# Kernel optimization log

Measured on AMD Instinct MI355X. Metric: run time of the kernel, lower is better.

The kernel has to match this reference:

```python
import jax, jax.numpy as jnp
import numpy as np

C = 128      # in channels
CO = 64      # out channels
G = 32       # group-norm groups
RES_IN = 32  # input resolution
RES_OUT = 64 # subdivided resolution
N = 20000    # active input voxels
EPS = 1e-5


def setup_inputs() -> dict:
    key = jax.random.key(0)
    ks = jax.random.split(key, 12)
    # unique active voxel coords at RES_IN (batch index 0, single instance)
    rng = np.random.default_rng(0)
    flat = rng.choice(RES_IN ** 3, size=N, replace=False)
    xyz = np.stack([flat // (RES_IN * RES_IN), (flat // RES_IN) % RES_IN, flat % RES_IN], axis=1)
    x_coords = jnp.asarray(np.concatenate([np.zeros((N, 1), np.int32), xyz.astype(np.int32)], axis=1))
    x_feats = jax.random.normal(ks[0], (N, C), dtype=jnp.float32)
    gn1_g = 1.0 + 0.1 * jax.random.normal(ks[1], (C,), dtype=jnp.float32)
    gn1_b = 0.1 * jax.random.normal(ks[2], (C,), dtype=jnp.float32)
    W1 = 0.05 * jax.random.normal(ks[3], (3, 3, 3, C, CO), dtype=jnp.float32)
    b1 = 0.01 * jax.random.normal(ks[4], (CO,), dtype=jnp.float32)
    gn2_g = 1.0 + 0.1 * jax.random.normal(ks[5], (CO,), dtype=jnp.float32)
    gn2_b = 0.1 * jax.random.normal(ks[6], (CO,), dtype=jnp.float32)
    W2 = 0.05 * jax.random.normal(ks[7], (3, 3, 3, CO, CO), dtype=jnp.float32)  # zero_module in source; random here to exercise math
    b2 = 0.01 * jax.random.normal(ks[8], (CO,), dtype=jnp.float32)
    Ws = 0.05 * jax.random.normal(ks[9], (C, CO), dtype=jnp.float32)   # 1x1 skip conv
    bs = 0.01 * jax.random.normal(ks[10], (CO,), dtype=jnp.float32)
    return dict(x_feats=x_feats, x_coords=x_coords, gn1_g=gn1_g, gn1_b=gn1_b,
                W1=W1, b1=b1, gn2_g=gn2_g, gn2_b=gn2_b, W2=W2, b2=b2, Ws=Ws, bs=bs)


def group_norm(f, g, b):
    # single-instance sparse group norm: stats per group over all points
    n, c = f.shape
    x = f.reshape(n, G, c // G)
    mu = jnp.mean(x, axis=(0, 2), keepdims=True)
    var = jnp.mean((x - mu) ** 2, axis=(0, 2), keepdims=True)
    return ((x - mu) * jax.lax.rsqrt(var + EPS)).reshape(n, c) * g + b


def subdivide(coords, feats):
    n = coords.shape[0]
    offs = jnp.stack(jnp.meshgrid(jnp.arange(2), jnp.arange(2), jnp.arange(2), indexing='ij'), -1).reshape(8, 3)
    xyz = coords[:, None, 1:] * 2 + offs[None].astype(coords.dtype)          # [n,8,3]
    bidx = jnp.broadcast_to(coords[:, None, :1], (n, 8, 1))
    new_coords = jnp.concatenate([bidx, xyz], axis=-1).reshape(n * 8, 4)
    return new_coords, jnp.repeat(feats, 8, axis=0)


def subm_conv3(coords, feats, W, b):
    # submanifold 3x3x3 sparse conv: scatter to padded dense grid, gather 27 neighbors per active site
    cin = feats.shape[1]
    grid = jnp.zeros((RES_OUT + 2, RES_OUT + 2, RES_OUT + 2, cin), feats.dtype)
    grid = grid.at[coords[:, 1] + 1, coords[:, 2] + 1, coords[:, 3] + 1].set(feats)
    acc = jnp.zeros((feats.shape[0], W.shape[-1]), feats.dtype)
    for i in range(3):
        for j in range(3):
            for k in range(3):
                nb = grid[coords[:, 1] + i, coords[:, 2] + j, coords[:, 3] + k]  # [n, cin]
                acc = acc + nb @ W[i, j, k]
    return acc + b


def reference(x_feats, x_coords, gn1_g, gn1_b, W1, b1, gn2_g, gn2_b, W2, b2, Ws, bs):
    h = jax.nn.silu(group_norm(x_feats, gn1_g, gn1_b))
    hc, hf = subdivide(x_coords, h)
    _, xf = subdivide(x_coords, x_feats)
    hf = subm_conv3(hc, hf, W1, b1)
    hf = jax.nn.silu(group_norm(hf, gn2_g, gn2_b))
    hf = subm_conv3(hc, hf, W2, b2)
    out = hf + (xf @ Ws + bs)  # residual + 1x1 skip conv (out_channels != channels)
    return out
```

## Files before the change

### kernel.cpp

```cpp
#include <hip/hip_runtime.h>
#include <hip/hip_bf16.h>
#include <math.h>

#define N_PTS 20000
#define C_IN 128
#define C_OUT 64
#define M_PTS (N_PTS*8)
#define EPS 1e-5f

typedef __attribute__((ext_vector_type(8))) short short8;
typedef __attribute__((ext_vector_type(4))) float float4v;

__device__ __forceinline__ ushort f2bf(float f){
    unsigned int i = __float_as_uint(f);
    unsigned int r = i + 0x7fffu + ((i >> 16) & 1u);
    return (ushort)(r >> 16);
}
__device__ __forceinline__ float bf2f(ushort u){ return __uint_as_float(((unsigned int)u) << 16); }
__device__ __forceinline__ float silu(float z){ return z / (1.f + expf(-z)); }


__global__ void __launch_bounds__(256) prep_kernel(
    const float* __restrict__ W1, const float* __restrict__ W2,
    ushort* __restrict__ Wt1, ushort* __restrict__ Wt2,
    int* __restrict__ pg, ushort* __restrict__ h, ushort* __restrict__ h2,
    const float* __restrict__ x, float* __restrict__ stats)
{
    const int b = blockIdx.x, tid = threadIdx.x;
    if (b < 864){
        int idx = b * 256 + tid;
        int j = idx & 7, l = (idx >> 3) & 63, nb = (idx >> 9) & 3, kb = (idx >> 11) & 3, t = idx >> 13;
        int ci = kb * 32 + (l >> 4) * 8 + j, co = nb * 16 + (l & 15);
        Wt1[idx] = f2bf(W1[(t * C_IN + ci) * 64 + co]);
    } else if (b < 1296){
        int idx = (b - 864) * 256 + tid;
        int j = idx & 7, l = (idx >> 3) & 63, nb = (idx >> 9) & 3, kb = (idx >> 11) & 1, t = idx >> 12;
        int ci = kb * 32 + (l >> 4) * 8 + j, co = nb * 16 + (l & 15);
        Wt2[idx] = f2bf(W2[(t * C_OUT + ci) * 64 + co]);
    } else if (b < 1424){
        int i = (b - 1296) * 256 + tid;
        pg[i] = -1;
        if (b == 1296){
            if (tid < C_IN) h[(size_t)N_PTS * C_IN + tid] = 0;
            if (tid < C_OUT) h2[(size_t)M_PTS * C_OUT + tid] = 0;
        }
    } else {
        __shared__ float ls[64];
        if (tid < 64) ls[tid] = 0.f;
        __syncthreads();
        const int g = tid & 31;
        const int r0 = (b - 1424) * 8 + (tid >> 5);
        float sum = 0.f, sq = 0.f;
        for (int r = r0; r < N_PTS; r += 4096){
            float4 v = *(const float4*)(x + (size_t)r * C_IN + g * 4);
            sum += v.x + v.y + v.z + v.w;
            sq  += v.x*v.x + v.y*v.y + v.z*v.z + v.w*v.w;
        }
        atomicAdd(&ls[g], sum);
        atomicAdd(&ls[32 + g], sq);
        __syncthreads();
        if (tid < 64) atomicAdd(&stats[tid], ls[tid]);
    }
}

__global__ void __launch_bounds__(256) mid_kernel(
    const int* __restrict__ cds, int* __restrict__ pg,
    const float* __restrict__ x, const float* __restrict__ stats,
    const float* __restrict__ g1, const float* __restrict__ b1, ushort* __restrict__ h,
    const float* __restrict__ Wsk, const float* __restrict__ bsk, float* __restrict__ s)
{
    __shared__ float w[C_IN * C_OUT];
    const int b = blockIdx.x, tid = threadIdx.x;
    if (b < 79){
        int i = b * 256 + tid;
        if (i < N_PTS){
            const int* cd = cds + i * 4;
            pg[(cd[1] * 32 + cd[2]) * 32 + cd[3]] = i;
        }
    } else if (b < 2579){
        int i = ((b - 79) * 256 + tid) * 4;
        int c0 = i & (C_IN - 1);
        int g = c0 >> 2;
        float mu = stats[g] * (1.0f / (N_PTS * 4.0f));
        float var = stats[32 + g] * (1.0f / (N_PTS * 4.0f)) - mu * mu;
        float rs = rsqrtf(var + EPS);
        float4 v = *(const float4*)(x + i);
        ushort4 o;
        o.x = f2bf(silu((v.x - mu) * rs * g1[c0+0] + b1[c0+0]));
        o.y = f2bf(silu((v.y - mu) * rs * g1[c0+1] + b1[c0+1]));
        o.z = f2bf(silu((v.z - mu) * rs * g1[c0+2] + b1[c0+2]));
        o.w = f2bf(silu((v.w - mu) * rs * g1[c0+3] + b1[c0+3]));
        *(ushort4*)(h + i) = o;
    } else {
        for (int j = tid; j < C_IN * C_OUT; j += 256) w[j] = Wsk[j];
        __syncthreads();
        int co = tid & 63, pr = tid >> 6;
        int p = (b - 2579) * 4 + pr;
        const float* xr = x + (size_t)p * C_IN;
        float a = bsk[co];
        for (int cb = 0; cb < C_IN; cb += 4){
            float4 v = *(const float4*)(xr + cb);
            a += v.x * w[(cb+0)*64+co] + v.y * w[(cb+1)*64+co]
               + v.z * w[(cb+2)*64+co] + v.w * w[(cb+3)*64+co];
        }
        s[(size_t)p * C_OUT + co] = a;
    }
}

template<int CIN, int CHILD>
__global__ void __launch_bounds__(64, 3) conv_direct(
    const ushort* __restrict__ feat, const int* __restrict__ pg,
    const int* __restrict__ coords, const ushort* __restrict__ Wt,
    const float* __restrict__ bias, const float* __restrict__ skip,
    ushort* __restrict__ hf1_bf, float* __restrict__ out, float* __restrict__ statsAcc)
{
    constexpr int KB = CIN / 32;
    __shared__ int rws[64];
    const int l = threadIdx.x;
    const int r16 = l & 15, qd = l >> 4;
    const int mb = blockIdx.x * 64;

    int cx0, cy0, cz0;
    {
        int m = mb + l, p = m >> 3, o = m & 7;
        cx0 = 2 * coords[p*4+1] + ((o >> 2) & 1);
        cy0 = 2 * coords[p*4+2] + ((o >> 1) & 1);
        cz0 = 2 * coords[p*4+3] + (o & 1);
    }

    float4v acc[4][4];
#pragma unroll
    for (int rb = 0; rb < 4; rb++)
#pragma unroll
        for (int nb = 0; nb < 4; nb++)
#pragma unroll
            for (int rg = 0; rg < 4; rg++) acc[rb][nb][rg] = 0.f;

    for (int t = 0; t < 27; t++){
        const int dx = t / 9 - 1, dy = (t / 3) % 3 - 1, dz = t % 3 - 1;
        const int cx = cx0 + dx, cy = cy0 + dy, cz = cz0 + dz;
        int row = 8 * N_PTS;
        if ((unsigned)cx < 64u && (unsigned)cy < 64u && (unsigned)cz < 64u){
            int pidx = pg[((cx >> 1) * 32 + (cy >> 1)) * 32 + (cz >> 1)];
            if (pidx >= 0) row = pidx * 8 + (((cx & 1) << 2) | ((cy & 1) << 1) | (cz & 1));
        }
        rws[l] = row;
        __syncthreads();
        int fr0 = rws[r16], fr1 = rws[16 + r16], fr2 = rws[32 + r16], fr3 = rws[48 + r16];
        if (!CHILD){ fr0 >>= 3; fr1 >>= 3; fr2 >>= 3; fr3 >>= 3; }
        const ushort* a0 = feat + (size_t)fr0 * CIN + qd * 8;
        const ushort* a1 = feat + (size_t)fr1 * CIN + qd * 8;
        const ushort* a2 = feat + (size_t)fr2 * CIN + qd * 8;
        const ushort* a3 = feat + (size_t)fr3 * CIN + qd * 8;
        const ushort* wt = Wt + (size_t)t * (KB * 2048) + l * 8;
#pragma unroll
        for (int kb = 0; kb < KB; kb++){
            short8 b0 = *(const short8*)(wt + (kb*4+0)*512);
            short8 b1 = *(const short8*)(wt + (kb*4+1)*512);
            short8 b2 = *(const short8*)(wt + (kb*4+2)*512);
            short8 b3 = *(const short8*)(wt + (kb*4+3)*512);
            short8 av0 = *(const short8*)(a0 + kb*32);
            short8 av1 = *(const short8*)(a1 + kb*32);
            short8 av2 = *(const short8*)(a2 + kb*32);
            short8 av3 = *(const short8*)(a3 + kb*32);
            acc[0][0] = __builtin_amdgcn_mfma_f32_16x16x32_bf16(av0, b0, acc[0][0], 0, 0, 0);
            acc[0][1] = __builtin_amdgcn_mfma_f32_16x16x32_bf16(av0, b1, acc[0][1], 0, 0, 0);
            acc[0][2] = __builtin_amdgcn_mfma_f32_16x16x32_bf16(av0, b2, acc[0][2], 0, 0, 0);
            acc[0][3] = __builtin_amdgcn_mfma_f32_16x16x32_bf16(av0, b3, acc[0][3], 0, 0, 0);
            acc[1][0] = __builtin_amdgcn_mfma_f32_16x16x32_bf16(av1, b0, acc[1][0], 0, 0, 0);
            acc[1][1] = __builtin_amdgcn_mfma_f32_16x16x32_bf16(av1, b1, acc[1][1], 0, 0, 0);
            acc[1][2] = __builtin_amdgcn_mfma_f32_16x16x32_bf16(av1, b2, acc[1][2], 0, 0, 0);
            acc[1][3] = __builtin_amdgcn_mfma_f32_16x16x32_bf16(av1, b3, acc[1][3], 0, 0, 0);
            acc[2][0] = __builtin_amdgcn_mfma_f32_16x16x32_bf16(av2, b0, acc[2][0], 0, 0, 0);
            acc[2][1] = __builtin_amdgcn_mfma_f32_16x16x32_bf16(av2, b1, acc[2][1], 0, 0, 0);
            acc[2][2] = __builtin_amdgcn_mfma_f32_16x16x32_bf16(av2, b2, acc[2][2], 0, 0, 0);
            acc[2][3] = __builtin_amdgcn_mfma_f32_16x16x32_bf16(av2, b3, acc[2][3], 0, 0, 0);
            acc[3][0] = __builtin_amdgcn_mfma_f32_16x16x32_bf16(av3, b0, acc[3][0], 0, 0, 0);
            acc[3][1] = __builtin_amdgcn_mfma_f32_16x16x32_bf16(av3, b1, acc[3][1], 0, 0, 0);
            acc[3][2] = __builtin_amdgcn_mfma_f32_16x16x32_bf16(av3, b2, acc[3][2], 0, 0, 0);
            acc[3][3] = __builtin_amdgcn_mfma_f32_16x16x32_bf16(av3, b3, acc[3][3], 0, 0, 0);
        }
    }

    float bsv[4] = { bias[r16], bias[16 + r16], bias[32 + r16], bias[48 + r16] };
    if (!CHILD){
        float ps[4] = {0,0,0,0}, pq[4] = {0,0,0,0};
#pragma unroll
        for (int rb = 0; rb < 4; rb++)
#pragma unroll
            for (int nb = 0; nb < 4; nb++)
#pragma unroll
                for (int rg = 0; rg < 4; rg++){
                    int mm = mb + rb * 16 + qd * 4 + rg;
                    float v = acc[rb][nb][rg] + bsv[nb];
                    hf1_bf[(size_t)mm * 64 + nb * 16 + r16] = f2bf(v);
                    ps[nb] += v; pq[nb] += v * v;
                }
#pragma unroll
        for (int nb = 0; nb < 4; nb++){
            float s1 = ps[nb], s2 = pq[nb];
            s1 += __shfl_xor(s1, 16, 64); s2 += __shfl_xor(s2, 16, 64);
            s1 += __shfl_xor(s1, 32, 64); s2 += __shfl_xor(s2, 32, 64);
            if (qd == 0){
                atomicAdd(&statsAcc[64 + nb * 16 + r16], s1);
                atomicAdd(&statsAcc[128 + nb * 16 + r16], s2);
            }
        }
    } else {
#pragma unroll
        for (int rb = 0; rb < 4; rb++)
#pragma unroll
            for (int rg = 0; rg < 4; rg++){
                int mm = mb + rb * 16 + qd * 4 + rg;
                const float* sk = skip + (size_t)(mm >> 3) * 64;
#pragma unroll
                for (int nb = 0; nb < 4; nb++){
                    int co = nb * 16 + r16;
                    out[(size_t)mm * 64 + co] = acc[rb][nb][rg] + bsv[nb] + sk[co];
                }
            }
    }
}

__global__ void __launch_bounds__(256) h2_kernel(
    const ushort* __restrict__ hf1, const float* __restrict__ stats,
    const float* __restrict__ gg, const float* __restrict__ gb, ushort* __restrict__ h2)
{
    int i = (blockIdx.x * 256 + threadIdx.x) * 4;
    if (i >= M_PTS * C_OUT) return;
    int c0 = i & (C_OUT - 1);
    const float inv = 1.0f / (M_PTS * 2.0f);
    float muA = (stats[64 + c0] + stats[64 + c0 + 1]) * inv;
    float vA  = (stats[128 + c0] + stats[128 + c0 + 1]) * inv - muA * muA;
    float rsA = rsqrtf(vA + EPS);
    float muB = (stats[64 + c0 + 2] + stats[64 + c0 + 3]) * inv;
    float vB  = (stats[128 + c0 + 2] + stats[128 + c0 + 3]) * inv - muB * muB;
    float rsB = rsqrtf(vB + EPS);
    ushort4 u = *(const ushort4*)(hf1 + i);
    ushort4 o;
    o.x = f2bf(silu((bf2f(u.x) - muA) * rsA * gg[c0+0] + gb[c0+0]));
    o.y = f2bf(silu((bf2f(u.y) - muA) * rsA * gg[c0+1] + gb[c0+1]));
    o.z = f2bf(silu((bf2f(u.z) - muB) * rsB * gg[c0+2] + gb[c0+2]));
    o.w = f2bf(silu((bf2f(u.w) - muB) * rsB * gg[c0+3] + gb[c0+3]));
    *(ushort4*)(h2 + i) = o;
}

extern "C" void kernel_launch(void* const* d_in, const int* in_sizes, int n_in,
                              void* d_out, int out_size, void* d_ws, size_t ws_size,
                              hipStream_t stream){
    const float* x   = (const float*)d_in[0];
    const int*   cds = (const int*)  d_in[1];
    const float* g1  = (const float*)d_in[2];
    const float* b1  = (const float*)d_in[3];
    const float* W1  = (const float*)d_in[4];
    const float* bb1 = (const float*)d_in[5];
    const float* g2  = (const float*)d_in[6];
    const float* b2  = (const float*)d_in[7];
    const float* W2  = (const float*)d_in[8];
    const float* bb2 = (const float*)d_in[9];
    const float* Wsk = (const float*)d_in[10];
    const float* bsk = (const float*)d_in[11];
    float* out = (float*)d_out;
    char* ws = (char*)d_ws;

    float*  stats = (float*) (ws);
    int*    pg    = (int*)   (ws + 1024);
    ushort* h     = (ushort*)(ws + 132096);
    ushort* h2    = (ushort*)(ws + 5252352);
    float*  s     = (float*) (ws + 25732480);
    ushort* Wt1   = (ushort*)(ws + 30852480);
    ushort* Wt2   = (ushort*)(ws + 31294848);

    hipMemsetAsync(stats, 0, 192 * sizeof(float), stream);
    prep_kernel<<<1936, 256, 0, stream>>>(W1, W2, Wt1, Wt2, pg, h, h2, x, stats);
    mid_kernel<<<7579, 256, 0, stream>>>(cds, pg, x, stats, g1, b1, h, Wsk, bsk, s);
    conv_direct<C_IN, 0><<<2500, 64, 0, stream>>>(h, pg, cds, Wt1, bb1, nullptr,
                                                  (ushort*)d_out, nullptr, stats);
    h2_kernel<<<12500, 256, 0, stream>>>((const ushort*)d_out, stats, g2, b2, h2);
    conv_direct<C_OUT, 1><<<2500, 64, 0, stream>>>(h2, pg, cds, Wt2, bb2, s,
                                                   nullptr, out, nullptr);
}
```

Baseline: 387.3 us.

## Halve conv tile to 32 rows and compute neighbor rows per lane without LDS sync

The sparse conv kernel now handles 32 output rows per 64-thread block instead of 64, which halves the accumulator registers and doubles the grid size. Each lane computes the neighbor rows it needs directly, so the LDS exchange and the per-tap __syncthreads go away, and the 27-tap loop is fully unrolled. The aim is higher occupancy (launch bounds raised to 4) and no barrier stalls. In exchange each weight fragment is reused across half as many rows, which doubles weight loads per output, and each lane repeats the hash-grid lookups.

```diff
diff --git a/kernel.cpp b/kernel.cpp
--- a/kernel.cpp
+++ b/kernel.cpp
@@ -108,50 +108,60 @@
 }
 
 template<int CIN, int CHILD>
-__global__ void __launch_bounds__(64, 3) conv_direct(
+__global__ void __launch_bounds__(64, 4) conv_direct(
     const ushort* __restrict__ feat, const int* __restrict__ pg,
     const int* __restrict__ coords, const ushort* __restrict__ Wt,
     const float* __restrict__ bias, const float* __restrict__ skip,
     ushort* __restrict__ hf1_bf, float* __restrict__ out, float* __restrict__ statsAcc)
 {
     constexpr int KB = CIN / 32;
-    __shared__ int rws[64];
+    constexpr int ZROW = CHILD ? (8 * N_PTS) : N_PTS;
     const int l = threadIdx.x;
     const int r16 = l & 15, qd = l >> 4;
-    const int mb = blockIdx.x * 64;
-
-    int cx0, cy0, cz0;
+    const int mb = blockIdx.x * 32;
+
+    int cxa, cya, cza, cxb, cyb, czb;
     {
-        int m = mb + l, p = m >> 3, o = m & 7;
-        cx0 = 2 * coords[p*4+1] + ((o >> 2) & 1);
-        cy0 = 2 * coords[p*4+2] + ((o >> 1) & 1);
-        cz0 = 2 * coords[p*4+3] + (o & 1);
-    }
-
-    float4v acc[4][4];
-#pragma unroll
-    for (int rb = 0; rb < 4; rb++)
+        int m = mb + r16, p = m >> 3, o = m & 7;
+        cxa = 2 * coords[p*4+1] + ((o >> 2) & 1);
+        cya = 2 * coords[p*4+2] + ((o >> 1) & 1);
+        cza = 2 * coords[p*4+3] + (o & 1);
+        m = mb + 16 + r16; p = m >> 3; o = m & 7;
+        cxb = 2 * coords[p*4+1] + ((o >> 2) & 1);
+        cyb = 2 * coords[p*4+2] + ((o >> 1) & 1);
+        czb = 2 * coords[p*4+3] + (o & 1);
+    }
+
+    float4v acc[2][4];
+#pragma unroll
+    for (int rb = 0; rb < 2; rb++)
 #pragma unroll
         for (int nb = 0; nb < 4; nb++)
 #pragma unroll
             for (int rg = 0; rg < 4; rg++) acc[rb][nb][rg] = 0.f;
 
+#pragma unroll
     for (int t = 0; t < 27; t++){
         const int dx = t / 9 - 1, dy = (t / 3) % 3 - 1, dz = t % 3 - 1;
-        const int cx = cx0 + dx, cy = cy0 + dy, cz = cz0 + dz;
-        int row = 8 * N_PTS;
-        if ((unsigned)cx < 64u && (unsigned)cy < 64u && (unsigned)cz < 64u){
-            int pidx = pg[((cx >> 1) * 32 + (cy >> 1)) * 32 + (cz >> 1)];
-            if (pidx >= 0) row = pidx * 8 + (((cx & 1) << 2) | ((cy & 1) << 1) | (cz & 1));
-        }
-        rws[l] = row;
-        __syncthreads();
-        int fr0 = rws[r16], fr1 = rws[16 + r16], fr2 = rws[32 + r16], fr3 = rws[48 + r16];
-        if (!CHILD){ fr0 >>= 3; fr1 >>= 3; fr2 >>= 3; fr3 >>= 3; }
+        int fr0 = ZROW, fr1 = ZROW;
+        {
+            int cx = cxa + dx, cy = cya + dy, cz = cza + dz;
+            if ((unsigned)(cx | cy | cz) < 64u){
+                int pidx = pg[(cx >> 1) * 1024 + (cy >> 1) * 32 + (cz >> 1)];
+                if (pidx >= 0)
+                    fr0 = CHILD ? pidx * 8 + (((cx & 1) << 2) | ((cy & 1) << 1) | (cz & 1))
+                                : pidx;
+            }
+            cx = cxb + dx; cy = cyb + dy; cz = czb + dz;
+            if ((unsigned)(cx | cy | cz) < 64u){
+                int pidx = pg[(cx >> 1) * 1024 + (cy >> 1) * 32 + (cz >> 1)];
+                if (pidx >= 0)
+                    fr1 = CHILD ? pidx * 8 + (((cx & 1) << 2) | ((cy & 1) << 1) | (cz & 1))
+                                : pidx;
+            }
+        }
         const ushort* a0 = feat + (size_t)fr0 * CIN + qd * 8;
         const ushort* a1 = feat + (size_t)fr1 * CIN + qd * 8;
-        const ushort* a2 = feat + (size_t)fr2 * CIN + qd * 8;
-        const ushort* a3 = feat + (size_t)fr3 * CIN + qd * 8;
         const ushort* wt = Wt + (size_t)t * (KB * 2048) + l * 8;
 #pragma unroll
         for (int kb = 0; kb < KB; kb++){
@@ -161,8 +171,6 @@
             short8 b3 = *(const short8*)(wt + (kb*4+3)*512);
             short8 av0 = *(const short8*)(a0 + kb*32);
             short8 av1 = *(const short8*)(a1 + kb*32);
-            short8 av2 = *(const short8*)(a2 + kb*32);
-            short8 av3 = *(const short8*)(a3 + kb*32);
             acc[0][0] = __builtin_amdgcn_mfma_f32_16x16x32_bf16(av0, b0, acc[0][0], 0, 0, 0);
             acc[0][1] = __builtin_amdgcn_mfma_f32_16x16x32_bf16(av0, b1, acc[0][1], 0, 0, 0);
             acc[0][2] = __builtin_amdgcn_mfma_f32_16x16x32_bf16(av0, b2, acc[0][2], 0, 0, 0);
@@ -171,14 +179,6 @@
             acc[1][1] = __builtin_amdgcn_mfma_f32_16x16x32_bf16(av1, b1, acc[1][1], 0, 0, 0);
             acc[1][2] = __builtin_amdgcn_mfma_f32_16x16x32_bf16(av1, b2, acc[1][2], 0, 0, 0);
             acc[1][3] = __builtin_amdgcn_mfma_f32_16x16x32_bf16(av1, b3, acc[1][3], 0, 0, 0);
-            acc[2][0] = __builtin_amdgcn_mfma_f32_16x16x32_bf16(av2, b0, acc[2][0], 0, 0, 0);
-            acc[2][1] = __builtin_amdgcn_mfma_f32_16x16x32_bf16(av2, b1, acc[2][1], 0, 0, 0);
-            acc[2][2] = __builtin_amdgcn_mfma_f32_16x16x32_bf16(av2, b2, acc[2][2], 0, 0, 0);
-            acc[2][3] = __builtin_amdgcn_mfma_f32_16x16x32_bf16(av2, b3, acc[2][3], 0, 0, 0);
-            acc[3][0] = __builtin_amdgcn_mfma_f32_16x16x32_bf16(av3, b0, acc[3][0], 0, 0, 0);
-            acc[3][1] = __builtin_amdgcn_mfma_f32_16x16x32_bf16(av3, b1, acc[3][1], 0, 0, 0);
-            acc[3][2] = __builtin_amdgcn_mfma_f32_16x16x32_bf16(av3, b2, acc[3][2], 0, 0, 0);
-            acc[3][3] = __builtin_amdgcn_mfma_f32_16x16x32_bf16(av3, b3, acc[3][3], 0, 0, 0);
         }
     }
 
@@ -186,7 +186,7 @@
     if (!CHILD){
         float ps[4] = {0,0,0,0}, pq[4] = {0,0,0,0};
 #pragma unroll
-        for (int rb = 0; rb < 4; rb++)
+        for (int rb = 0; rb < 2; rb++)
 #pragma unroll
             for (int nb = 0; nb < 4; nb++)
 #pragma unroll
@@ -208,7 +208,7 @@
         }
     } else {
 #pragma unroll
-        for (int rb = 0; rb < 4; rb++)
+        for (int rb = 0; rb < 2; rb++)
 #pragma unroll
             for (int rg = 0; rg < 4; rg++){
                 int mm = mb + rb * 16 + qd * 4 + rg;
@@ -274,9 +274,9 @@
     hipMemsetAsync(stats, 0, 192 * sizeof(float), stream);
     prep_kernel<<<1936, 256, 0, stream>>>(W1, W2, Wt1, Wt2, pg, h, h2, x, stats);
     mid_kernel<<<7579, 256, 0, stream>>>(cds, pg, x, stats, g1, b1, h, Wsk, bsk, s);
-    conv_direct<C_IN, 0><<<2500, 64, 0, stream>>>(h, pg, cds, Wt1, bb1, nullptr,
+    conv_direct<C_IN, 0><<<5000, 64, 0, stream>>>(h, pg, cds, Wt1, bb1, nullptr,
                                                   (ushort*)d_out, nullptr, stats);
     h2_kernel<<<12500, 256, 0, stream>>>((const ushort*)d_out, stats, g2, b2, h2);
-    conv_direct<C_OUT, 1><<<2500, 64, 0, stream>>>(h2, pg, cds, Wt2, bb2, s,
+    conv_direct<C_OUT, 1><<<5000, 64, 0, stream>>>(h2, pg, cds, Wt2, bb2, s,
                                                    nullptr, out, nullptr);
 }
```

Result: slower. 525.9 us (+35.8%).
